# Kernel optimization log

Measured on AMD Instinct MI355X. Metric: run time of the kernel, lower is better.

The kernel has to match this reference:

```python
import jax, jax.numpy as jnp
import numpy as np

B, C, CI, H, W = 4, 256, 128, 64, 64  # batch, in_channels, inter_channels, spatial


def conv1x1(x, w, b):
    # x: [B,C,H,W], w: [O,C], b: [O] -> [B,O,H,W]
    return jnp.einsum('bchw,oc->bohw', x, w) + b[None, :, None, None]


def setup_inputs() -> dict:
    key = jax.random.key(0)
    ks = jax.random.split(key, 9)
    s = 0.02
    return {
        'x':  jax.random.normal(ks[0], (B, C, H, W), dtype=jnp.float32),
        'Wg': jax.random.normal(ks[1], (CI, C), dtype=jnp.float32) * s,
        'bg': jnp.zeros((CI,), dtype=jnp.float32),
        'Wt': jax.random.normal(ks[2], (CI, C), dtype=jnp.float32) * s,
        'bt': jnp.zeros((CI,), dtype=jnp.float32),
        'Wp': jax.random.normal(ks[3], (CI, C), dtype=jnp.float32) * s,
        'bp': jnp.zeros((CI,), dtype=jnp.float32),
        'Wo': jax.random.normal(ks[4], (C, CI), dtype=jnp.float32) * s,
        'bo': jnp.zeros((C,), dtype=jnp.float32),
    }


def reference(x, Wg, bg, Wt, bt, Wp, bp, Wo, bo):
    b, c, h, w = x.shape
    n = h * w
    g  = conv1x1(x, Wg, bg).reshape(b, -1, n)   # [B,CI,N]
    th = conv1x1(x, Wt, bt).reshape(b, -1, n)   # [B,CI,N]
    ph = conv1x1(x, Wp, bp).reshape(b, -1, n)   # [B,CI,N]
    f = jnp.einsum('bci,bcj->bij', th, ph)      # [B,N,N] unscaled scores
    a = jax.nn.softmax(f, axis=-1)
    y = jnp.einsum('bij,bcj->bci', a, g)        # [B,CI,N]
    y = y.reshape(b, -1, h, w)
    return conv1x1(y, Wo, bo) + x
```

## Files before the change

### kernel.cpp

```cpp
#include <hip/hip_runtime.h>
#include <math.h>

#define B_  4
#define C_  256
#define CI_ 128
#define N_  4096

typedef short s16x8  __attribute__((ext_vector_type(8)));
typedef float f32x4  __attribute__((ext_vector_type(4)));
typedef float f32x16 __attribute__((ext_vector_type(16)));

__device__ inline ushort f2bf(float f) {
    unsigned int u = __float_as_uint(f);
    u += 0x7FFF + ((u >> 16) & 1);
    return (ushort)(u >> 16);
}
__device__ inline float bf2f(ushort u) {
    return __uint_as_float(((unsigned int)u) << 16);
}

__device__ inline unsigned pkbf(float a, float b) {
    unsigned r;
    asm("v_cvt_pk_bf16_f32 %0, %1, %2" : "=v"(r) : "v"(a), "v"(b));
    return r;
}
__device__ inline void plswap(unsigned &x, unsigned &y) {
    asm volatile("v_permlane32_swap_b32 %0, %1" : "+v"(x), "+v"(y));
}
__device__ inline float fexp2(float x) {
    float r;
    asm("v_exp_f32 %0, %1" : "=v"(r) : "v"(x));
    return r;
}

__device__ inline void gload_lds16(const void* g, void* l) {
    __builtin_amdgcn_global_load_lds(
        (const __attribute__((address_space(1))) unsigned int*)g,
        (__attribute__((address_space(3))) unsigned int*)l, 16, 0, 0);
}

__device__ inline void block_sync_lds() {
    asm volatile("s_waitcnt lgkmcnt(0)" ::: "memory");
    __builtin_amdgcn_s_barrier();
    asm volatile("" ::: "memory");
}

#define LOG2E 1.44269504f

__global__ __launch_bounds__(256) void prep_kernel(
    const float* __restrict__ Wg, const float* __restrict__ Wt,
    const float* __restrict__ Wp, const float* __restrict__ Wo,
    const float* __restrict__ bg, const float* __restrict__ bt,
    const float* __restrict__ bp,
    ushort* __restrict__ Wcat, ushort* __restrict__ Wobf,
    float* __restrict__ bcat,
    const float* __restrict__ x, ushort* __restrict__ xT)
{
    __shared__ ushort Ls[64][72];
    const int bid = blockIdx.x;
    const int t = threadIdx.x;
    if (bid < 512) {
        int i = bid * 256 + t;
        if (i < 32768)       Wcat[i] = f2bf(Wg[i]);
        else if (i < 65536)  Wcat[i] = f2bf(Wt[i - 32768]);
        else if (i < 98304)  Wcat[i] = f2bf(Wp[i - 65536]);
        else if (i < 131072) Wobf[i - 98304] = f2bf(Wo[i - 98304]);
        if (i < 128)         bcat[i] = bg[i];
        else if (i < 256)    bcat[i] = bt[i - 128];
        else if (i < 384)    bcat[i] = bp[i - 256];
        return;
    }
    int idx2 = bid - 512;
    const int n0 = (idx2 & 63) * 64;
    const int c0 = ((idx2 >> 6) & 3) * 64;
    const int b  = idx2 >> 8;
    const float* xb = x + ((size_t)b * C_ + c0) * N_ + n0;
    #pragma unroll
    for (int r = 0; r < 4; r++) {
        int idx = t + 256 * r;
        int c = idx >> 4, n4 = (idx & 15) * 4;
        float4 v = *(const float4*)&xb[(size_t)c * N_ + n4];
        ushort4 o;
        o.x = f2bf(v.x); o.y = f2bf(v.y); o.z = f2bf(v.z); o.w = f2bf(v.w);
        *(ushort4*)&Ls[c][n4] = o;
    }
    __syncthreads();
    ushort* xTb = xT + ((size_t)b * N_ + n0) * C_ + c0;
    #pragma unroll
    for (int r = 0; r < 2; r++) {
        int idx = t + 256 * r;
        int n = idx >> 3, c8 = (idx & 7) * 8;
        ushort tmp[8];
        #pragma unroll
        for (int u = 0; u < 8; u++) tmp[u] = Ls[c8 + u][n];
        *(uint4*)&xTb[(size_t)n * C_ + c8] = *(uint4*)tmp;
    }
}

__global__ __launch_bounds__(256, 2) void proj_kernel(
    const ushort* __restrict__ Wcat, const float* __restrict__ bcat,
    const ushort* __restrict__ xT,
    ushort* __restrict__ g, ushort* __restrict__ tht, ushort* __restrict__ pht)
{
    __shared__ __align__(16) char smem[65536];
    const int b = blockIdx.z, mt = blockIdx.y, n0 = blockIdx.x * 128;
    const int t = threadIdx.x, wv = t >> 6, lane = t & 63;
    const int wr = wv >> 1, wc = wv & 1;
    const int g4 = lane >> 4, ln = lane & 15;

    const char* Asrc = (const char*)(Wcat + (size_t)mt * 128 * C_);
    const char* Bsrc = (const char*)(xT + ((size_t)b * N_ + n0) * C_);

    const int sr = lane >> 3;
    const int sc = (lane & 7) << 4;
    const int ssw = sc ^ (sr << 4);

    f32x4 acc[4][4];
    #pragma unroll
    for (int i = 0; i < 4; i++)
        #pragma unroll
        for (int j = 0; j < 4; j++) acc[i][j] = (f32x4){0.f, 0.f, 0.f, 0.f};

    const int rsw = (ln & 7) << 4;

#define PROJ_STAGE(bufofs, k0) do {                                          \
    _Pragma("unroll")                                                        \
    for (int r_ = 0; r_ < 4; r_++) {                                         \
        int c_   = (wv << 2) + r_;                                           \
        int row_ = (c_ << 3) + sr;                                           \
        gload_lds16(Asrc + (size_t)row_ * 512 + (k0) * 2 + ssw,              \
                    smem + (bufofs) + (c_ << 10));                           \
        gload_lds16(Bsrc + (size_t)row_ * 512 + (k0) * 2 + ssw,              \
                    smem + (bufofs) + 16384 + (c_ << 10));                   \
    }                                                                        \
} while (0)

    PROJ_STAGE(0, 0);
    int buf = 0;
    #pragma unroll
    for (int s = 0; s < 4; s++) {
        if (s < 3) {
            PROJ_STAGE(buf ^ 32768, (s + 1) * 64);
            asm volatile("s_waitcnt vmcnt(8)" ::: "memory");
        } else {
            asm volatile("s_waitcnt vmcnt(0)" ::: "memory");
        }
        __builtin_amdgcn_s_barrier();
        asm volatile("" ::: "memory");

        const char* Ab = smem + buf;
        const char* Bb = smem + buf + 16384;
        #pragma unroll
        for (int kk = 0; kk < 2; kk++) {
            s16x8 aW[4], bX[4];
            #pragma unroll
            for (int m4 = 0; m4 < 4; m4++)
                aW[m4] = *(const s16x8*)(Ab + ((wr * 64 + m4 * 16 + ln) << 7)
                                            + (((kk << 6) + (g4 << 4)) ^ rsw));
            #pragma unroll
            for (int nt = 0; nt < 4; nt++)
                bX[nt] = *(const s16x8*)(Bb + ((wc * 64 + nt * 16 + ln) << 7)
                                            + (((kk << 6) + (g4 << 4)) ^ rsw));
            __builtin_amdgcn_s_setprio(1);
            #pragma unroll
            for (int m4 = 0; m4 < 4; m4++)
                #pragma unroll
                for (int nt = 0; nt < 4; nt++)
                    acc[m4][nt] = __builtin_amdgcn_mfma_f32_16x16x32_bf16(
                        aW[m4], bX[nt], acc[m4][nt], 0, 0, 0);
            __builtin_amdgcn_s_setprio(0);
        }
        block_sync_lds();
        buf ^= 32768;
    }

    if (mt == 0) {
        ushort* ob = g + (size_t)b * CI_ * N_;
        #pragma unroll
        for (int m4 = 0; m4 < 4; m4++) {
            #pragma unroll
            for (int r = 0; r < 4; r++) {
                int m = wr * 64 + m4 * 16 + 4 * g4 + r;
                float bi = bcat[m];
                #pragma unroll
                for (int nt = 0; nt < 4; nt++) {
                    int n = n0 + wc * 64 + nt * 16 + ln;
                    ob[(size_t)m * N_ + n] = f2bf(acc[m4][nt][r] + bi);
                }
            }
        }
    } else {
        ushort* ob = (mt == 1 ? tht : pht) + (size_t)b * N_ * CI_;
        const float* bb = bcat + mt * 128;
        const float scale = (mt == 1) ? LOG2E : 1.0f;
        #pragma unroll
        for (int m4 = 0; m4 < 4; m4++) {
            int mbase = wr * 64 + m4 * 16 + 4 * g4;
            #pragma unroll
            for (int nt = 0; nt < 4; nt++) {
                int n = n0 + wc * 64 + nt * 16 + ln;
                ushort v4[4];
                #pragma unroll
                for (int r = 0; r < 4; r++)
                    v4[r] = f2bf((acc[m4][nt][r] + bb[mbase + r]) * scale);
                *(ushort4*)&ob[(size_t)n * CI_ + mbase] = *(ushort4*)v4;
            }
        }
    }
#undef PROJ_STAGE
}


__device__ inline float build_pa(const f32x16& S, s16x8& f0, s16x8& f1) {
    float e[16];
    #pragma unroll
    for (int i = 0; i < 16; i++) e[i] = fexp2(S[i]);
    float t0[8];
    #pragma unroll
    for (int i = 0; i < 8; i++) t0[i] = e[2 * i] + e[2 * i + 1];
    float t1a = (t0[0] + t0[1]) + (t0[2] + t0[3]);
    float t1b = (t0[4] + t0[5]) + (t0[6] + t0[7]);
    float ls = t1a + t1b;
    unsigned w[8];
    #pragma unroll
    for (int i = 0; i < 8; i++) w[i] = pkbf(e[2 * i], e[2 * i + 1]);
    plswap(w[0], w[2]);
    plswap(w[1], w[3]);
    plswap(w[4], w[6]);
    plswap(w[5], w[7]);
    union { unsigned u[4]; s16x8 v; } A, B;
    A.u[0] = w[0]; A.u[1] = w[1]; A.u[2] = w[2]; A.u[3] = w[3];
    B.u[0] = w[4]; B.u[1] = w[5]; B.u[2] = w[6]; B.u[3] = w[7];
    f0 = A.v; f1 = B.v;
    return ls;
}

#define STAGE_KV(bufofs, jsrc) do {                                          \
    _Pragma("unroll")                                                        \
    for (int r_ = 0; r_ < 4; r_++) {                                         \
        int c_   = (wv << 2) + r_;                                           \
        int row_ = (c_ << 2) + srw;                                          \
        int so_  = slt ^ (row_ & 15);                                        \
        gload_lds16(kB + (((jsrc) + row_) << 8) + (so_ << 4),                \
                    smemB + (bufofs) + (c_ << 10));                          \
    }                                                                        \
    _Pragma("unroll")                                                        \
    for (int r_ = 0; r_ < 4; r_++) {                                         \
        int c_   = (wv << 2) + r_;                                           \
        int rr_  = (c_ << 2) + srw;                                          \
        int so_  = slt ^ (rr_ & 15);                                         \
        int d_   = (rr_ << 1) + (so_ >> 3);                                  \
        gload_lds16(vB + (size_t)d_ * (N_ * 2) + ((jsrc) << 1) + ((so_ & 7) << 4), \
                    smemB + (bufofs) + 16384 + (c_ << 10));                  \
    }                                                                        \
} while (0)

#define NC_ 4
#define JC_ (N_ / NC_)

__global__ __launch_bounds__(256, 2) void attn_mfma_kernel(
    const ushort* __restrict__ qn,
    const ushort* __restrict__ kn,
    const ushort* __restrict__ vm,
    ushort* __restrict__ Opart,
    float* __restrict__ lbuf)
{
    __shared__ __align__(16) char smemB[65536];

    constexpr int NI = N_ / 128;
    constexpr int nb = NI * NC_ * B_;
    int flat = (blockIdx.z * NC_ + blockIdx.y) * NI + blockIdx.x;
    int nf   = (flat & 7) * (nb / 8) + (flat >> 3);
    const int i0    = (nf % NI) * 128;
    const int chunk = (nf / NI) % NC_;
    const int b     = nf / (NI * NC_);
    const int jbase = chunk * JC_;

    const int t    = threadIdx.x;
    const int wv   = t >> 6;
    const int lane = t & 63;
    const int n32  = lane & 31;
    const int h    = lane >> 5;

    const int kswz = (n32 & 15) << 4;
    const int vswz = ((n32 >> 1) & 15) << 4;

    const char* kB = (const char*)(kn + (size_t)b * N_ * CI_);
    const char* vB = (const char*)(vm + (size_t)b * CI_ * N_);

    const ushort* qb = qn + ((size_t)b * N_ + i0) * CI_;
    s16x8 aQ[8];
    #pragma unroll
    for (int kk = 0; kk < 8; kk++)
        aQ[kk] = *(const s16x8*)(qb + (size_t)(32 * wv + n32) * CI_ + 16 * kk + 8 * h);

    f32x16 Oacc[4];
    #pragma unroll
    for (int dt = 0; dt < 4; dt++)
        #pragma unroll
        for (int e = 0; e < 16; e++) Oacc[dt][e] = 0.f;
    float lsum = 0.f;

    const int srw = lane >> 4;
    const int slt = lane & 15;

    STAGE_KV(0, jbase);
    int buf = 0;
    for (int jt = jbase; jt < jbase + JC_; jt += 64) {
        if (jt + 64 < jbase + JC_) {
            STAGE_KV(buf ^ 32768, jt + 64);
            asm volatile("s_waitcnt vmcnt(8)" ::: "memory");
        } else {
            asm volatile("s_waitcnt vmcnt(0)" ::: "memory");
        }
        __builtin_amdgcn_s_barrier();
        asm volatile("" ::: "memory");

        const char* Kc = smemB + buf;
        const char* Vc = smemB + buf + 16384;

        s16x8 pa[4];
        {
            f32x16 S0;
            #pragma unroll
            for (int e = 0; e < 16; e++) S0[e] = 0.f;
            __builtin_amdgcn_s_setprio(1);
            #pragma unroll
            for (int kk = 0; kk < 8; kk++) {
                s16x8 aK = *(const s16x8*)(Kc + (n32 << 8)
                                              + (((kk << 5) + (h << 4)) ^ kswz));
                S0 = __builtin_amdgcn_mfma_f32_32x32x16_bf16(aK, aQ[kk], S0, 0, 0, 0);
            }
            __builtin_amdgcn_s_setprio(0);
            lsum += build_pa(S0, pa[0], pa[1]);
        }
        {
            f32x16 S1;
            #pragma unroll
            for (int e = 0; e < 16; e++) S1[e] = 0.f;
            __builtin_amdgcn_s_setprio(1);
            #pragma unroll
            for (int kk = 0; kk < 8; kk++) {
                s16x8 aK = *(const s16x8*)(Kc + ((32 + n32) << 8)
                                              + (((kk << 5) + (h << 4)) ^ kswz));
                S1 = __builtin_amdgcn_mfma_f32_32x32x16_bf16(aK, aQ[kk], S1, 0, 0, 0);
            }
            __builtin_amdgcn_s_setprio(0);
            lsum += build_pa(S1, pa[2], pa[3]);
        }

        __builtin_amdgcn_s_setprio(1);
        #pragma unroll
        for (int dt = 0; dt < 4; dt++) {
            int vrow = (dt << 4) + (n32 >> 1);
            #pragma unroll
            for (int kk = 0; kk < 4; kk++) {
                s16x8 bV = *(const s16x8*)(Vc + (vrow << 8)
                    + ((((n32 & 1) << 7) + (kk << 5) + (h << 4)) ^ vswz));
                Oacc[dt] = __builtin_amdgcn_mfma_f32_32x32x16_bf16(pa[kk], bV, Oacc[dt], 0, 0, 0);
            }
        }
        __builtin_amdgcn_s_setprio(0);

        block_sync_lds();
        buf ^= 32768;
    }

    ushort* Ob = Opart + (size_t)chunk * (B_ * N_ * CI_) + ((size_t)b * N_ + i0) * CI_;
    #pragma unroll
    for (int rg = 0; rg < 16; rg++) {
        int R = (rg & 3) + 8 * (rg >> 2) + 4 * h;
        int q = 32 * wv + R;
        #pragma unroll
        for (int dt = 0; dt < 4; dt++)
            Ob[(size_t)q * CI_ + 32 * dt + n32] = f2bf(Oacc[dt][rg]);
    }
    float ot  = __shfl_xor(lsum, 32);
    float tot = lsum + ot;
    if (h == 0)
        lbuf[((size_t)chunk * B_ + b) * N_ + i0 + 32 * wv + n32] = tot;
}

__global__ __launch_bounds__(256, 2) void outgemm_kernel(
    const ushort* __restrict__ Wobf, const float* __restrict__ bo,
    const ushort* __restrict__ Opart, const float* __restrict__ lbuf,
    const float* __restrict__ x, float* __restrict__ out)
{
    __shared__ __align__(16) char smem[65536];
    __shared__ float invL[128];
    const int b = blockIdx.z, m0 = blockIdx.y * 128, n0 = blockIdx.x * 128;
    const int t = threadIdx.x, wv = t >> 6, lane = t & 63;
    const int wr = wv >> 1, wc = wv & 1;
    const int g4 = lane >> 4, ln = lane & 15;
    const size_t cs = (size_t)B_ * N_ * CI_;

    {
        const char* Wsrc = (const char*)(Wobf + (size_t)m0 * CI_);
        int srl = lane >> 4;
        int scl = (lane & 15) << 4;
        #pragma unroll
        for (int r = 0; r < 8; r++) {
            int c   = (wv << 3) + r;
            int row = (c << 2) + srl;
            gload_lds16(Wsrc + (size_t)row * 256 + (scl ^ ((row & 15) << 4)),
                        smem + (c << 10));
        }
    }

    if (t < 128) {
        float ls = 0.f;
        #pragma unroll
        for (int c = 0; c < NC_; c++)
            ls += lbuf[((size_t)c * B_ + b) * N_ + n0 + t];
        invL[t] = 1.0f / ls;
    }
    block_sync_lds();

    {
        #pragma unroll
        for (int r = 0; r < 8; r++) {
            int c   = t + 256 * r;
            int row = c >> 4;
            int col = (c & 15) << 4;
            size_t obase = ((size_t)b * N_ + n0 + row) * CI_ + (c & 15) * 8;
            float inv = invL[row];
            float osum[8];
            #pragma unroll
            for (int u = 0; u < 8; u++) osum[u] = 0.f;
            #pragma unroll
            for (int cc = 0; cc < NC_; cc++) {
                ushort oc[8];
                *(uint4*)oc = *(const uint4*)&Opart[(size_t)cc * cs + obase];
                #pragma unroll
                for (int u = 0; u < 8; u++) osum[u] += bf2f(oc[u]);
            }
            ushort yo[8];
            #pragma unroll
            for (int u = 0; u < 8; u++) yo[u] = f2bf(osum[u] * inv);
            *(uint4*)(smem + 32768 + row * 256 + (col ^ ((row & 15) << 4))) = *(uint4*)yo;
        }
    }
    asm volatile("s_waitcnt vmcnt(0)" ::: "memory");
    block_sync_lds();

    f32x4 acc[4][4];
    #pragma unroll
    for (int i = 0; i < 4; i++)
        #pragma unroll
        for (int j = 0; j < 4; j++) acc[i][j] = (f32x4){0.f, 0.f, 0.f, 0.f};

    const int rsw = ln << 4;
    #pragma unroll
    for (int kk = 0; kk < 4; kk++) {
        s16x8 aW[4], bY[4];
        #pragma unroll
        for (int m4 = 0; m4 < 4; m4++)
            aW[m4] = *(const s16x8*)(smem + ((wr * 64 + m4 * 16 + ln) << 8)
                                          + (((kk << 6) + (g4 << 4)) ^ rsw));
        #pragma unroll
        for (int nt = 0; nt < 4; nt++)
            bY[nt] = *(const s16x8*)(smem + 32768 + ((wc * 64 + nt * 16 + ln) << 8)
                                          + (((kk << 6) + (g4 << 4)) ^ rsw));
        __builtin_amdgcn_s_setprio(1);
        #pragma unroll
        for (int m4 = 0; m4 < 4; m4++)
            #pragma unroll
            for (int nt = 0; nt < 4; nt++)
                acc[m4][nt] = __builtin_amdgcn_mfma_f32_16x16x32_bf16(
                    aW[m4], bY[nt], acc[m4][nt], 0, 0, 0);
        __builtin_amdgcn_s_setprio(0);
    }

    float* outb = out + (size_t)b * C_ * N_;
    const float* xb = x + (size_t)b * C_ * N_;
    #pragma unroll
    for (int m4 = 0; m4 < 4; m4++) {
        #pragma unroll
        for (int r = 0; r < 4; r++) {
            int m = m0 + wr * 64 + m4 * 16 + 4 * g4 + r;
            float bi = bo[m];
            #pragma unroll
            for (int nt = 0; nt < 4; nt++) {
                size_t idx = (size_t)m * N_ + n0 + wc * 64 + nt * 16 + ln;
                outb[idx] = acc[m4][nt][r] + bi + xb[idx];
            }
        }
    }
}

extern "C" void kernel_launch(void* const* d_in, const int* in_sizes, int n_in,
                              void* d_out, int out_size, void* d_ws, size_t ws_size,
                              hipStream_t stream) {
    const float* x  = (const float*)d_in[0];
    const float* Wg = (const float*)d_in[1];
    const float* bg = (const float*)d_in[2];
    const float* Wt = (const float*)d_in[3];
    const float* bt = (const float*)d_in[4];
    const float* Wp = (const float*)d_in[5];
    const float* bp = (const float*)d_in[6];
    const float* Wo = (const float*)d_in[7];
    const float* bo = (const float*)d_in[8];
    float* out = (float*)d_out;

    char* w = (char*)d_ws;
    ushort* xT    = (ushort*)w;
    ushort* Opart = (ushort*)w;
    ushort* g     = (ushort*)(w + 16777216);
    ushort* tht   = (ushort*)(w + 20971520);
    ushort* pht   = (ushort*)(w + 25165824);
    ushort* Wcat  = (ushort*)(w + 29360128);
    ushort* Wobf  = (ushort*)(w + 29556736);
    float*  bcat  = (float*) (w + 29622272);
    float*  lbuf  = (float*) (w + 29623808);

    dim3 blk(256);
    prep_kernel<<<1536, blk, 0, stream>>>(Wg, Wt, Wp, Wo, bg, bt, bp,
                                          Wcat, Wobf, bcat, x, xT);
    proj_kernel<<<dim3(N_ / 128, 3, B_), blk, 0, stream>>>(Wcat, bcat, xT, g, tht, pht);
    attn_mfma_kernel<<<dim3(N_ / 128, NC_, B_), blk, 0, stream>>>(tht, pht, g, Opart, lbuf);
    outgemm_kernel<<<dim3(N_ / 128, C_ / 128, B_), blk, 0, stream>>>(Wobf, bo, Opart, lbuf, x, out);
}
```

Baseline: 141.4 us.

## Double query rows per warp to reuse K/V tiles, add 8-way split when workspace allows

Each warp now handles 64 query rows instead of 32, so every K and V fragment read from LDS feeds two MFMAs. This halves LDS traffic per unit of MFMA work and halves the number of times K/V are staged per query row. The grid in the query dimension is halved. To keep enough blocks in flight, the key dimension is split into 8 chunks when the workspace is large enough, at the cost of more partial-output traffic in the reduction GEMM. Register pressure roughly doubles for the accumulators and Q fragments, which may lower occupancy or cause spills.

```diff
diff --git a/kernel.cpp b/kernel.cpp
--- a/kernel.cpp
+++ b/kernel.cpp
@@ -255,9 +255,7 @@
     }                                                                        \
 } while (0)
 
-#define NC_ 4
-#define JC_ (N_ / NC_)
-
+template <int NC>
 __global__ __launch_bounds__(256, 2) void attn_mfma_kernel(
     const ushort* __restrict__ qn,
     const ushort* __restrict__ kn,
@@ -265,16 +263,17 @@
     ushort* __restrict__ Opart,
     float* __restrict__ lbuf)
 {
+    constexpr int JC = N_ / NC;
     __shared__ __align__(16) char smemB[65536];
 
-    constexpr int NI = N_ / 128;
-    constexpr int nb = NI * NC_ * B_;
-    int flat = (blockIdx.z * NC_ + blockIdx.y) * NI + blockIdx.x;
+    constexpr int NI = N_ / 256;
+    constexpr int nb = NI * NC * B_;
+    int flat = (blockIdx.z * NC + blockIdx.y) * NI + blockIdx.x;
     int nf   = (flat & 7) * (nb / 8) + (flat >> 3);
-    const int i0    = (nf % NI) * 128;
-    const int chunk = (nf / NI) % NC_;
-    const int b     = nf / (NI * NC_);
-    const int jbase = chunk * JC_;
+    const int i0    = (nf % NI) * 256;
+    const int chunk = (nf / NI) % NC;
+    const int b     = nf / (NI * NC);
+    const int jbase = chunk * JC;
 
     const int t    = threadIdx.x;
     const int wv   = t >> 6;
@@ -288,26 +287,28 @@
     const char* kB = (const char*)(kn + (size_t)b * N_ * CI_);
     const char* vB = (const char*)(vm + (size_t)b * CI_ * N_);
 
-    const ushort* qb = qn + ((size_t)b * N_ + i0) * CI_;
-    s16x8 aQ[8];
-    #pragma unroll
-    for (int kk = 0; kk < 8; kk++)
-        aQ[kk] = *(const s16x8*)(qb + (size_t)(32 * wv + n32) * CI_ + 16 * kk + 8 * h);
-
-    f32x16 Oacc[4];
+    const ushort* qbw = qn + ((size_t)b * N_ + i0 + 64 * wv) * CI_;
+    s16x8 aQA[8], aQB[8];
+    #pragma unroll
+    for (int kk = 0; kk < 8; kk++) {
+        aQA[kk] = *(const s16x8*)(qbw + (size_t)n32 * CI_ + 16 * kk + 8 * h);
+        aQB[kk] = *(const s16x8*)(qbw + (size_t)(32 + n32) * CI_ + 16 * kk + 8 * h);
+    }
+
+    f32x16 OA[4], OB[4];
     #pragma unroll
     for (int dt = 0; dt < 4; dt++)
         #pragma unroll
-        for (int e = 0; e < 16; e++) Oacc[dt][e] = 0.f;
-    float lsum = 0.f;
+        for (int e = 0; e < 16; e++) { OA[dt][e] = 0.f; OB[dt][e] = 0.f; }
+    float lsA = 0.f, lsB = 0.f;
 
     const int srw = lane >> 4;
     const int slt = lane & 15;
 
     STAGE_KV(0, jbase);
     int buf = 0;
-    for (int jt = jbase; jt < jbase + JC_; jt += 64) {
-        if (jt + 64 < jbase + JC_) {
+    for (int jt = jbase; jt < jbase + JC; jt += 64) {
+        if (jt + 64 < jbase + JC) {
             STAGE_KV(buf ^ 32768, jt + 64);
             asm volatile("s_waitcnt vmcnt(8)" ::: "memory");
         } else {
@@ -319,68 +320,68 @@
         const char* Kc = smemB + buf;
         const char* Vc = smemB + buf + 16384;
 
-        s16x8 pa[4];
-        {
-            f32x16 S0;
-            #pragma unroll
-            for (int e = 0; e < 16; e++) S0[e] = 0.f;
+        #pragma unroll
+        for (int half = 0; half < 2; half++) {
+            f32x16 SA, SB;
+            #pragma unroll
+            for (int e = 0; e < 16; e++) { SA[e] = 0.f; SB[e] = 0.f; }
             __builtin_amdgcn_s_setprio(1);
             #pragma unroll
             for (int kk = 0; kk < 8; kk++) {
-                s16x8 aK = *(const s16x8*)(Kc + (n32 << 8)
+                s16x8 aK = *(const s16x8*)(Kc + ((half * 32 + n32) << 8)
                                               + (((kk << 5) + (h << 4)) ^ kswz));
-                S0 = __builtin_amdgcn_mfma_f32_32x32x16_bf16(aK, aQ[kk], S0, 0, 0, 0);
+                SA = __builtin_amdgcn_mfma_f32_32x32x16_bf16(aK, aQA[kk], SA, 0, 0, 0);
+                SB = __builtin_amdgcn_mfma_f32_32x32x16_bf16(aK, aQB[kk], SB, 0, 0, 0);
             }
             __builtin_amdgcn_s_setprio(0);
-            lsum += build_pa(S0, pa[0], pa[1]);
-        }
-        {
-            f32x16 S1;
-            #pragma unroll
-            for (int e = 0; e < 16; e++) S1[e] = 0.f;
+
+            s16x8 pA0, pA1, pB0, pB1;
+            lsA += build_pa(SA, pA0, pA1);
+            lsB += build_pa(SB, pB0, pB1);
+
             __builtin_amdgcn_s_setprio(1);
             #pragma unroll
-            for (int kk = 0; kk < 8; kk++) {
-                s16x8 aK = *(const s16x8*)(Kc + ((32 + n32) << 8)
-                                              + (((kk << 5) + (h << 4)) ^ kswz));
-                S1 = __builtin_amdgcn_mfma_f32_32x32x16_bf16(aK, aQ[kk], S1, 0, 0, 0);
+            for (int dt = 0; dt < 4; dt++) {
+                int vrow = (dt << 4) + (n32 >> 1);
+                #pragma unroll
+                for (int k2 = 0; k2 < 2; k2++) {
+                    int kk = half * 2 + k2;
+                    s16x8 bV = *(const s16x8*)(Vc + (vrow << 8)
+                        + ((((n32 & 1) << 7) + (kk << 5) + (h << 4)) ^ vswz));
+                    OA[dt] = __builtin_amdgcn_mfma_f32_32x32x16_bf16(
+                        k2 == 0 ? pA0 : pA1, bV, OA[dt], 0, 0, 0);
+                    OB[dt] = __builtin_amdgcn_mfma_f32_32x32x16_bf16(
+                        k2 == 0 ? pB0 : pB1, bV, OB[dt], 0, 0, 0);
+                }
             }
             __builtin_amdgcn_s_setprio(0);
-            lsum += build_pa(S1, pa[2], pa[3]);
-        }
-
-        __builtin_amdgcn_s_setprio(1);
-        #pragma unroll
-        for (int dt = 0; dt < 4; dt++) {
-            int vrow = (dt << 4) + (n32 >> 1);
-            #pragma unroll
-            for (int kk = 0; kk < 4; kk++) {
-                s16x8 bV = *(const s16x8*)(Vc + (vrow << 8)
-                    + ((((n32 & 1) << 7) + (kk << 5) + (h << 4)) ^ vswz));
-                Oacc[dt] = __builtin_amdgcn_mfma_f32_32x32x16_bf16(pa[kk], bV, Oacc[dt], 0, 0, 0);
-            }
-        }
-        __builtin_amdgcn_s_setprio(0);
+        }
 
         block_sync_lds();
         buf ^= 32768;
     }
 
-    ushort* Ob = Opart + (size_t)chunk * (B_ * N_ * CI_) + ((size_t)b * N_ + i0) * CI_;
+    ushort* Ob = Opart + (size_t)chunk * (B_ * N_ * CI_)
+                       + ((size_t)b * N_ + i0 + 64 * wv) * CI_;
     #pragma unroll
     for (int rg = 0; rg < 16; rg++) {
         int R = (rg & 3) + 8 * (rg >> 2) + 4 * h;
-        int q = 32 * wv + R;
-        #pragma unroll
-        for (int dt = 0; dt < 4; dt++)
-            Ob[(size_t)q * CI_ + 32 * dt + n32] = f2bf(Oacc[dt][rg]);
-    }
-    float ot  = __shfl_xor(lsum, 32);
-    float tot = lsum + ot;
-    if (h == 0)
-        lbuf[((size_t)chunk * B_ + b) * N_ + i0 + 32 * wv + n32] = tot;
-}
-
+        #pragma unroll
+        for (int dt = 0; dt < 4; dt++) {
+            Ob[(size_t)R * CI_ + 32 * dt + n32]        = f2bf(OA[dt][rg]);
+            Ob[(size_t)(32 + R) * CI_ + 32 * dt + n32] = f2bf(OB[dt][rg]);
+        }
+    }
+    float totA = lsA + __shfl_xor(lsA, 32);
+    float totB = lsB + __shfl_xor(lsB, 32);
+    if (h == 0) {
+        float* lb = lbuf + ((size_t)chunk * B_ + b) * N_ + i0 + 64 * wv;
+        lb[n32]      = totA;
+        lb[32 + n32] = totB;
+    }
+}
+
+template <int NC>
 __global__ __launch_bounds__(256, 2) void outgemm_kernel(
     const ushort* __restrict__ Wobf, const float* __restrict__ bo,
     const ushort* __restrict__ Opart, const float* __restrict__ lbuf,
@@ -410,7 +411,7 @@
     if (t < 128) {
         float ls = 0.f;
         #pragma unroll
-        for (int c = 0; c < NC_; c++)
+        for (int c = 0; c < NC; c++)
             ls += lbuf[((size_t)c * B_ + b) * N_ + n0 + t];
         invL[t] = 1.0f / ls;
     }
@@ -428,7 +429,7 @@
             #pragma unroll
             for (int u = 0; u < 8; u++) osum[u] = 0.f;
             #pragma unroll
-            for (int cc = 0; cc < NC_; cc++) {
+            for (int cc = 0; cc < NC; cc++) {
                 ushort oc[8];
                 *(uint4*)oc = *(const uint4*)&Opart[(size_t)cc * cs + obase];
                 #pragma unroll
@@ -502,21 +503,30 @@
     const float* bo = (const float*)d_in[8];
     float* out = (float*)d_out;
 
+    const bool big = ws_size >= 46925312ull;
+    const int NC = big ? 8 : 4;
+
     char* w = (char*)d_ws;
+    size_t opart_sz = (size_t)NC * B_ * N_ * CI_ * sizeof(ushort);
     ushort* xT    = (ushort*)w;
     ushort* Opart = (ushort*)w;
-    ushort* g     = (ushort*)(w + 16777216);
-    ushort* tht   = (ushort*)(w + 20971520);
-    ushort* pht   = (ushort*)(w + 25165824);
-    ushort* Wcat  = (ushort*)(w + 29360128);
-    ushort* Wobf  = (ushort*)(w + 29556736);
-    float*  bcat  = (float*) (w + 29622272);
-    float*  lbuf  = (float*) (w + 29623808);
+    ushort* g     = (ushort*)(w + opart_sz);
+    ushort* tht   = (ushort*)(w + opart_sz + 4194304);
+    ushort* pht   = (ushort*)(w + opart_sz + 8388608);
+    ushort* Wcat  = (ushort*)(w + opart_sz + 12582912);
+    ushort* Wobf  = (ushort*)(w + opart_sz + 12582912 + 196608);
+    float*  bcat  = (float*) (w + opart_sz + 12582912 + 262144);
+    float*  lbuf  = (float*) (w + opart_sz + 12582912 + 263680);
 
     dim3 blk(256);
     prep_kernel<<<1536, blk, 0, stream>>>(Wg, Wt, Wp, Wo, bg, bt, bp,
                                           Wcat, Wobf, bcat, x, xT);
     proj_kernel<<<dim3(N_ / 128, 3, B_), blk, 0, stream>>>(Wcat, bcat, xT, g, tht, pht);
-    attn_mfma_kernel<<<dim3(N_ / 128, NC_, B_), blk, 0, stream>>>(tht, pht, g, Opart, lbuf);
-    outgemm_kernel<<<dim3(N_ / 128, C_ / 128, B_), blk, 0, stream>>>(Wobf, bo, Opart, lbuf, x, out);
-}
+    if (big) {
+        attn_mfma_kernel<8><<<dim3(N_ / 256, 8, B_), blk, 0, stream>>>(tht, pht, g, Opart, lbuf);
+        outgemm_kernel<8><<<dim3(N_ / 128, C_ / 128, B_), blk, 0, stream>>>(Wobf, bo, Opart, lbuf, x, out);
+    } else {
+        attn_mfma_kernel<4><<<dim3(N_ / 256, 4, B_), blk, 0, stream>>>(tht, pht, g, Opart, lbuf);
+        outgemm_kernel<4><<<dim3(N_ / 128, C_ / 128, B_), blk, 0, stream>>>(Wobf, bo, Opart, lbuf, x, out);
+    }
+}
```

Measured after the change: 205.8 us. 1.46x slower.
